# Performance work log

Hardware: AMD Instinct MI355X
Metric: run time of the kernel (lower is better)

## Reference

```python
import jax, jax.numpy as jnp
import numpy as np

MODES = 256
WIDTH = 64
T_HIST = 1
T_FUT = 1
BATCH = 64
S = 8192


def setup_inputs() -> dict:
    key = jax.random.key(0)
    ks = jax.random.split(key, 12)
    scale = 1.0 / (WIDTH * WIDTH)
    inp = {
        "u": jax.random.normal(ks[0], (BATCH, S, T_HIST), dtype=jnp.float32),
        # lifting layer: Linear(T_HIST+1 -> WIDTH), stored [in, out]
        "fc0_w": jax.random.normal(ks[1], (T_HIST + 1, WIDTH), dtype=jnp.float32) * 0.5,
        "fc0_b": jax.random.normal(ks[2], (WIDTH,), dtype=jnp.float32) * 0.1,
        # 4 spectral conv layers, complex weights stored as real/imag parts
        "sw_r": scale * jax.random.uniform(ks[3], (4, WIDTH, WIDTH, MODES), dtype=jnp.float32),
        "sw_i": scale * jax.random.uniform(ks[4], (4, WIDTH, WIDTH, MODES), dtype=jnp.float32),
        # 4 pointwise (1x1 conv) layers: weight [out,in], bias [out]
        "pw_w": jax.random.normal(ks[5], (4, WIDTH, WIDTH), dtype=jnp.float32) * (1.0 / np.sqrt(WIDTH)),
        "pw_b": jax.random.normal(ks[6], (4, WIDTH), dtype=jnp.float32) * 0.1,
        # projection head
        "fc1_w": jax.random.normal(ks[7], (WIDTH, 128), dtype=jnp.float32) * (1.0 / np.sqrt(WIDTH)),
        "fc1_b": jax.random.normal(ks[8], (128,), dtype=jnp.float32) * 0.1,
        "fc2_w": jax.random.normal(ks[9], (128, T_FUT), dtype=jnp.float32) * (1.0 / np.sqrt(128)),
        "fc2_b": jax.random.normal(ks[10], (T_FUT,), dtype=jnp.float32) * 0.1,
    }
    return inp


def _spectral_conv(x, wr, wi):
    # x: [b, c_in, s] real; weights: [c_in, c_out, MODES] (real/imag parts)
    s = x.shape[-1]
    xf = jnp.fft.rfft(x)                     # [b, c_in, s//2+1] complex
    w = wr + 1j * wi
    om = jnp.einsum('bix,iox->box', xf[:, :, :MODES], w)  # [b, c_out, MODES]
    out_ft = jnp.zeros((x.shape[0], wr.shape[1], s // 2 + 1), dtype=om.dtype)
    out_ft = out_ft.at[:, :, :MODES].set(om)
    return jnp.fft.irfft(out_ft, n=s)        # [b, c_out, s] real


def reference(u, fc0_w, fc0_b, sw_r, sw_i, pw_w, pw_b, fc1_w, fc1_b, fc2_w, fc2_b):
    b, s, _ = u.shape
    grid = jnp.broadcast_to(jnp.linspace(0.0, 1.0, s, dtype=u.dtype)[None, :, None], (b, s, 1))
    x = jnp.concatenate([u, grid], axis=-1)              # [b, s, 2]
    x = x @ fc0_w + fc0_b                                # [b, s, W]
    x = jnp.transpose(x, (0, 2, 1))                      # [b, W, s]
    for l in range(4):
        x1 = _spectral_conv(x, sw_r[l], sw_i[l])
        x2 = jnp.einsum('oi,bis->bos', pw_w[l], x) + pw_b[l][None, :, None]
        x = x1 + x2
        if l < 3:
            x = jax.nn.gelu(x, approximate=False)
    x = jnp.transpose(x, (0, 2, 1))                      # [b, s, W]
    x = jax.nn.gelu(x @ fc1_w + fc1_b, approximate=False)
    x = x @ fc2_w + fc2_b                                # [b, s, T_FUT]
    return x
```

## Files before the change

kernel.cpp:

```cpp
#include <hip/hip_runtime.h>
#include <hip/hip_bf16.h>
#include <math.h>

#define BB 64
#define CC 64
#define SS 8192
#define HS 4096
#define NMODE 256
#define KK2 512

typedef __attribute__((ext_vector_type(8))) short short8;
typedef __attribute__((ext_vector_type(16))) float f32x16;

__device__ __forceinline__ float gelu_exact(float v) {
    return 0.5f * v * (1.0f + erff(v * 0.7071067811865476f));
}
__device__ __forceinline__ float b2f(ushort u) {
    return __uint_as_float(((unsigned int)u) << 16);
}
__device__ __forceinline__ ushort f2b(float v) {
    __hip_bfloat16 h = __float2bfloat16(v);
    return *(ushort*)&h;
}
__device__ __forceinline__ void split2(float v, ushort& h, ushort& l) {
    h = f2b(v);
    l = f2b(v - b2f(h));
}
__device__ __forceinline__ int colk(int c) {
    return (c < 256) ? (c & ~1) : (((c - 256) & ~1) | 1);
}

__global__ void build_T1p(ushort* __restrict__ h, ushort* __restrict__ l) {
    int c = blockIdx.x;
    int n = blockIdx.y * 256 + threadIdx.x;
    int k = colk(c), ri = c & 1;
    int m = (n * k) & (SS - 1);
    float th = (float)m * (6.283185307179586476925f / (float)SS);
    float s, co;
    sincosf(th, &s, &co);
    float v = ri ? -s : co;
    ushort hh, ll;
    split2(v, hh, ll);
    h[(size_t)c * HS + n] = hh;
    l[(size_t)c * HS + n] = ll;
}

__global__ void build_T2r(ushort* __restrict__ h, ushort* __restrict__ l) {
    int n = blockIdx.x;
    int c = blockIdx.y * 256 + threadIdx.x;
    int k = colk(c), ri = c & 1;
    int m = (n * k) & (SS - 1);
    float th = (float)m * (6.283185307179586476925f / (float)SS);
    float s, co;
    sincosf(th, &s, &co);
    float v = ri ? -s : co;
    ushort hh, ll;
    split2(v, hh, ll);
    h[(size_t)n * KK2 + c] = hh;
    l[(size_t)n * KK2 + c] = ll;
}

__global__ void zero_xf(float* __restrict__ p) {
    size_t i = ((size_t)blockIdx.x * 256 + threadIdx.x) * 4;
    *(float4*)&p[i] = make_float4(0.f, 0.f, 0.f, 0.f);
}

__global__ void lift_kernel(const float* __restrict__ u, const float* __restrict__ w0,
                            const float* __restrict__ b0, ushort* __restrict__ Eh,
                            ushort* __restrict__ El, ushort* __restrict__ Oh,
                            ushort* __restrict__ Ol) {
    int n = blockIdx.x * 256 + threadIdx.x;
    int c = blockIdx.y;
    int b = blockIdx.z;
    float g1 = (float)n * (1.0f / (float)(SS - 1));
    float g2 = (float)(n + HS) * (1.0f / (float)(SS - 1));
    float v1 = u[b * SS + n] * w0[c] + g1 * w0[CC + c] + b0[c];
    float v2 = u[b * SS + n + HS] * w0[c] + g2 * w0[CC + c] + b0[c];
    float E = v1 + v2, O = v1 - v2;
    ushort hh, ll;
    size_t idx = (size_t)(b * CC + c) * HS + n;
    split2(E, hh, ll);
    Eh[idx] = hh;
    El[idx] = ll;
    split2(O, hh, ll);
    Oh[idx] = hh;
    Ol[idx] = ll;
}

__global__ __launch_bounds__(256, 3) void dft_mfma(
    const ushort* __restrict__ Eh, const ushort* __restrict__ El,
    const ushort* __restrict__ Oh, const ushort* __restrict__ Ol,
    const ushort* __restrict__ t1h, const ushort* __restrict__ t1l,
    float* __restrict__ Xf) {
    __shared__ __align__(16) ushort SM[16384];
    ushort* As_h = SM;
    ushort* As_l = SM + 4096;
    ushort* Bs_h = SM + 8192;
    ushort* Bs_l = SM + 12288;
    const int t = threadIdx.x;
    const int L = blockIdx.x;
    const int gq = L >> 5, j = L & 31;
    const int c0 = (j >> 3) * 128;
    const int m0 = ((gq & 3) * 8 + (j & 7)) * 128;
    const int kz = (gq >> 2) * 1024;
    const ushort* __restrict__ Ahp = (c0 < 256) ? Eh : Oh;
    const ushort* __restrict__ Alp = (c0 < 256) ? El : Ol;
    const int lane = t & 63, w = t >> 6;
    const int wm = (w >> 1) * 64, wn = (w & 1) * 64;
    const int l32 = lane & 31, lh = lane >> 5;
    const int sr = t >> 1, sh = (t & 1) * 16;
    const int g0 = (t & 1) * 2;
    const int d0 = ((g0 + 0) * 128 + sr) * 8;
    const int d1 = ((g0 + 1) * 128 + sr) * 8;

    f32x16 acc[2][2];
#pragma unroll
    for (int i = 0; i < 2; i++)
#pragma unroll
        for (int jj = 0; jj < 2; jj++) acc[i][jj] = (f32x16)0.f;

    const size_t arow = (size_t)(m0 + sr) * HS;
    const size_t brow = (size_t)(c0 + sr) * HS;
    const int kend = kz + 1024;

    short8 a0h, a1h, a0l, a1l, b0h, b1h, b0l, b1l;
    {
        const size_t ga = arow + kz + sh;
        const size_t gb = brow + kz + sh;
        a0h = *(const short8*)&Ahp[ga];
        a1h = *(const short8*)&Ahp[ga + 8];
        a0l = *(const short8*)&Alp[ga];
        a1l = *(const short8*)&Alp[ga + 8];
        b0h = *(const short8*)&t1h[gb];
        b1h = *(const short8*)&t1h[gb + 8];
        b0l = *(const short8*)&t1l[gb];
        b1l = *(const short8*)&t1l[gb + 8];
    }
    for (int kt = kz; kt < kend; kt += 32) {
        __syncthreads();
        *(short8*)&As_h[d0] = a0h;
        *(short8*)&As_h[d1] = a1h;
        *(short8*)&As_l[d0] = a0l;
        *(short8*)&As_l[d1] = a1l;
        *(short8*)&Bs_h[d0] = b0h;
        *(short8*)&Bs_h[d1] = b1h;
        *(short8*)&Bs_l[d0] = b0l;
        *(short8*)&Bs_l[d1] = b1l;
        __syncthreads();
        const int ktn = (kt + 32 < kend) ? kt + 32 : kz;
        const size_t ga = arow + ktn + sh;
        const size_t gb = brow + ktn + sh;
        a0h = *(const short8*)&Ahp[ga];
        a1h = *(const short8*)&Ahp[ga + 8];
        a0l = *(const short8*)&Alp[ga];
        a1l = *(const short8*)&Alp[ga + 8];
        b0h = *(const short8*)&t1h[gb];
        b1h = *(const short8*)&t1h[gb + 8];
        b0l = *(const short8*)&t1l[gb];
        b1l = *(const short8*)&t1l[gb + 8];
#pragma unroll
        for (int s2 = 0; s2 < 2; s2++) {
            const int kg = s2 * 2 + lh;
            short8 ah[2], al[2], bh2[2], bl2[2];
#pragma unroll
            for (int mt = 0; mt < 2; mt++) {
                int off = (kg * 128 + wm + mt * 32 + l32) * 8;
                ah[mt] = *(const short8*)&As_h[off];
                al[mt] = *(const short8*)&As_l[off];
            }
#pragma unroll
            for (int nt = 0; nt < 2; nt++) {
                int off = (kg * 128 + wn + nt * 32 + l32) * 8;
                bh2[nt] = *(const short8*)&Bs_h[off];
                bl2[nt] = *(const short8*)&Bs_l[off];
            }
#pragma unroll
            for (int nt = 0; nt < 2; nt++)
#pragma unroll
                for (int mt = 0; mt < 2; mt++) {
                    acc[mt][nt] = __builtin_amdgcn_mfma_f32_32x32x16_bf16(ah[mt], bh2[nt], acc[mt][nt], 0, 0, 0);
                    acc[mt][nt] = __builtin_amdgcn_mfma_f32_32x32x16_bf16(ah[mt], bl2[nt], acc[mt][nt], 0, 0, 0);
                    acc[mt][nt] = __builtin_amdgcn_mfma_f32_32x32x16_bf16(al[mt], bh2[nt], acc[mt][nt], 0, 0, 0);
                }
        }
    }
#pragma unroll
    for (int mt = 0; mt < 2; mt++)
#pragma unroll
        for (int nt = 0; nt < 2; nt++) {
            int col = c0 + wn + nt * 32 + l32;
#pragma unroll
            for (int reg = 0; reg < 16; reg++) {
                int row = m0 + wm + mt * 32 + (reg & 3) + 8 * (reg >> 2) + 4 * lh;
                atomicAdd(&Xf[(size_t)row * KK2 + col], acc[mt][nt][reg]);
            }
        }
}

__global__ __launch_bounds__(256) void mode_mix(const float* __restrict__ Xf,
                                                const float* __restrict__ swr,
                                                const float* __restrict__ swi,
                                                ushort* __restrict__ omh,
                                                ushort* __restrict__ oml, int l) {
    int k = threadIdx.x;
    int bg = blockIdx.x * 2;
    int og = blockIdx.y * 2;
    const int cp = ((k & 1) << 8) | ((k >> 1) << 1);
    float ar[2][2] = {}, ai[2][2] = {};
#pragma unroll 2
    for (int i = 0; i < CC; i++) {
        float2 x0 = *(const float2*)&Xf[((size_t)(bg + 0) * CC + i) * KK2 + cp];
        float2 x1 = *(const float2*)&Xf[((size_t)(bg + 1) * CC + i) * KK2 + cp];
        size_t wb = ((size_t)(l * CC + i) * CC + og) * NMODE + k;
        float wr0 = swr[wb], wi0 = swi[wb];
        float wr1 = swr[wb + NMODE], wi1 = swi[wb + NMODE];
        ar[0][0] += x0.x * wr0 - x0.y * wi0;
        ai[0][0] += x0.x * wi0 + x0.y * wr0;
        ar[0][1] += x0.x * wr1 - x0.y * wi1;
        ai[0][1] += x0.x * wi1 + x0.y * wr1;
        ar[1][0] += x1.x * wr0 - x1.y * wi0;
        ai[1][0] += x1.x * wi0 + x1.y * wr0;
        ar[1][1] += x1.x * wr1 - x1.y * wi1;
        ai[1][1] += x1.x * wi1 + x1.y * wr1;
    }
    float ck = (k == 0) ? (1.0f / (float)SS) : (2.0f / (float)SS);
#pragma unroll
    for (int b2 = 0; b2 < 2; b2++)
#pragma unroll
        for (int oo = 0; oo < 2; oo++) {
            float re = ar[b2][oo] * ck;
            float im = ai[b2][oo] * ck;
            ushort hr, lr2, hi2, li2;
            split2(re, hr, lr2);
            split2(im, hi2, li2);
            size_t base = ((size_t)(bg + b2) * CC + og + oo) * KK2 + cp;
            *(ushort2*)&omh[base] = make_ushort2(hr, hi2);
            *(ushort2*)&oml[base] = make_ushort2(lr2, li2);
        }
}

__global__ __launch_bounds__(256, 3) void inv_mfma(
    const ushort* __restrict__ omh, const ushort* __restrict__ oml,
    const ushort* __restrict__ t2h, const ushort* __restrict__ t2l,
    const float* __restrict__ pww, const float* __restrict__ pwb,
    ushort* __restrict__ Eh, ushort* __restrict__ El,
    ushort* __restrict__ Oh, ushort* __restrict__ Ol, int l, int gel) {
    __shared__ __align__(16) ushort SM[12288];
    ushort* As_h = SM;
    ushort* As_l = SM + 4096;
    ushort* Bs_h = SM + 8192;
    ushort* Bs_l = SM + 10240;
    const int t = threadIdx.x;
    const int n0 = blockIdx.x * 64;
    const int row0 = blockIdx.y * 128;
    const int lane = t & 63, w = t >> 6;
    const int wm = (w >> 1) * 64, wn = (w & 1) * 32;
    const int l32 = lane & 31, lh = lane >> 5;
    const int sr = t >> 1, sh = (t & 1) * 16;
    const int g0 = (t & 1) * 2;
    const int dA0 = ((g0 + 0) * 128 + sr) * 8;
    const int dA1 = ((g0 + 1) * 128 + sr) * 8;
    const int srB = (t >> 1) & 63;
    const int dB0 = ((g0 + 0) * 64 + srB) * 8;
    const int dB1 = ((g0 + 1) * 64 + srB) * 8;
    const bool doB = t < 128;

    f32x16 aP[2], aQ[2];
#pragma unroll
    for (int i = 0; i < 2; i++) {
        aP[i] = (f32x16)0.f;
        aQ[i] = (f32x16)0.f;
    }

    const size_t arow = (size_t)(row0 + sr) * KK2;
    const size_t brow = (size_t)(n0 + srB) * KK2;

    short8 a0h, a1h, a0l, a1l, b0h, b1h, b0l, b1l;
    {
        const size_t ga = arow + sh;
        a0h = *(const short8*)&omh[ga];
        a1h = *(const short8*)&omh[ga + 8];
        a0l = *(const short8*)&oml[ga];
        a1l = *(const short8*)&oml[ga + 8];
        if (doB) {
            const size_t gb = brow + sh;
            b0h = *(const short8*)&t2h[gb];
            b1h = *(const short8*)&t2h[gb + 8];
            b0l = *(const short8*)&t2l[gb];
            b1l = *(const short8*)&t2l[gb + 8];
        }
    }
#pragma unroll
    for (int half = 0; half < 2; half++) {
        f32x16* acc = half ? aQ : aP;
        for (int hs8 = 0; hs8 < 8; hs8++) {
            const int hs = half * 8 + hs8;
            __syncthreads();
            *(short8*)&As_h[dA0] = a0h;
            *(short8*)&As_h[dA1] = a1h;
            *(short8*)&As_l[dA0] = a0l;
            *(short8*)&As_l[dA1] = a1l;
            if (doB) {
                *(short8*)&Bs_h[dB0] = b0h;
                *(short8*)&Bs_h[dB1] = b1h;
                *(short8*)&Bs_l[dB0] = b0l;
                *(short8*)&Bs_l[dB1] = b1l;
            }
            __syncthreads();
            const int ktn = (hs + 1 < 16) ? (hs + 1) * 32 : 0;
            const size_t ga = arow + ktn + sh;
            a0h = *(const short8*)&omh[ga];
            a1h = *(const short8*)&omh[ga + 8];
            a0l = *(const short8*)&oml[ga];
            a1l = *(const short8*)&oml[ga + 8];
            if (doB) {
                const size_t gb = brow + ktn + sh;
                b0h = *(const short8*)&t2h[gb];
                b1h = *(const short8*)&t2h[gb + 8];
                b0l = *(const short8*)&t2l[gb];
                b1l = *(const short8*)&t2l[gb + 8];
            }
#pragma unroll
            for (int s2 = 0; s2 < 2; s2++) {
                const int kg = s2 * 2 + lh;
                short8 ah[2], al[2];
#pragma unroll
                for (int mt = 0; mt < 2; mt++) {
                    int off = (kg * 128 + wm + mt * 32 + l32) * 8;
                    ah[mt] = *(const short8*)&As_h[off];
                    al[mt] = *(const short8*)&As_l[off];
                }
                const int offb = (kg * 64 + wn + l32) * 8;
                short8 bh = *(const short8*)&Bs_h[offb];
                short8 bl = *(const short8*)&Bs_l[offb];
#pragma unroll
                for (int mt = 0; mt < 2; mt++) {
                    acc[mt] = __builtin_amdgcn_mfma_f32_32x32x16_bf16(ah[mt], bh, acc[mt], 0, 0, 0);
                    acc[mt] = __builtin_amdgcn_mfma_f32_32x32x16_bf16(ah[mt], bl, acc[mt], 0, 0, 0);
                    acc[mt] = __builtin_amdgcn_mfma_f32_32x32x16_bf16(al[mt], bh, acc[mt], 0, 0, 0);
                }
            }
        }
    }
#pragma unroll
    for (int mt = 0; mt < 2; mt++) {
        f32x16 p = aP[mt];
        aP[mt] = p + aQ[mt];
        aQ[mt] = p - aQ[mt];
    }
    const int bsw = w >> 1;
    const int xbs = t >> 7, xi = (t >> 1) & 63, xseg = (t & 1) * 32;
    const size_t xg = (size_t)(row0 + xbs * 64 + xi) * HS + n0 + xseg;
    const ushort* const srcs[4] = {Eh, El, Oh, Ol};
#pragma unroll
    for (int r = 0; r < 4; r++) {
        const ushort* src = srcs[r];
        const bool isO = (r >= 2), isHi = !(r & 1);
        short8 v0 = *(const short8*)&src[xg];
        short8 v1 = *(const short8*)&src[xg + 8];
        short8 v2 = *(const short8*)&src[xg + 16];
        short8 v3 = *(const short8*)&src[xg + 24];
        __syncthreads();
        {
            ushort* d = &SM[xbs * 4608 + xi * 72 + xseg];
            *(short8*)d = v0;
            *(short8*)(d + 8) = v1;
            *(short8*)(d + 16) = v2;
            *(short8*)(d + 24) = v3;
        }
        __syncthreads();
#pragma unroll
        for (int ks = 0; ks < 4; ks++) {
            short8 pah[2], pal[2], pnh[2], pnl[2];
#pragma unroll
            for (int mt = 0; mt < 2; mt++) {
                int o = mt * 32 + l32;
                const float* pp = &pww[(size_t)(l * CC + o) * CC + ks * 16 + lh * 8];
                float4 pa = *(const float4*)pp;
                float4 pb = *(const float4*)(pp + 4);
                float pv[8] = {pa.x, pa.y, pa.z, pa.w, pb.x, pb.y, pb.z, pb.w};
#pragma unroll
                for (int e = 0; e < 8; e++) {
                    ushort h2, l2;
                    split2(0.5f * pv[e], h2, l2);
                    pah[mt][e] = (short)h2;
                    pal[mt][e] = (short)l2;
                    pnh[mt][e] = (short)(h2 ^ 0x8000);
                    pnl[mt][e] = (short)(l2 ^ 0x8000);
                }
            }
            short8 bf;
            const int rb = bsw * 4608 + (ks * 16 + lh * 8) * 72 + wn + l32;
#pragma unroll
            for (int jj = 0; jj < 8; jj++) bf[jj] = (short)SM[rb + jj * 72];
#pragma unroll
            for (int mt = 0; mt < 2; mt++) {
                aP[mt] = __builtin_amdgcn_mfma_f32_32x32x16_bf16(pah[mt], bf, aP[mt], 0, 0, 0);
                aQ[mt] = __builtin_amdgcn_mfma_f32_32x32x16_bf16(isO ? pnh[mt] : pah[mt], bf, aQ[mt], 0, 0, 0);
                if (isHi) {
                    aP[mt] = __builtin_amdgcn_mfma_f32_32x32x16_bf16(pal[mt], bf, aP[mt], 0, 0, 0);
                    aQ[mt] = __builtin_amdgcn_mfma_f32_32x32x16_bf16(isO ? pnl[mt] : pal[mt], bf, aQ[mt], 0, 0, 0);
                }
            }
        }
    }
#pragma unroll
    for (int mt = 0; mt < 2; mt++)
#pragma unroll
        for (int reg = 0; reg < 16; reg++) {
            int roffs = (reg & 3) + 8 * (reg >> 2) + 4 * lh;
            int o = mt * 32 + roffs;
            float bias = pwb[l * CC + o];
            float uu = aP[mt][reg] + bias;
            float vv = aQ[mt][reg] + bias;
            if (gel) {
                uu = gelu_exact(uu);
                vv = gelu_exact(vv);
            }
            float EE = uu + vv, OO = uu - vv;
            ushort h2, l2;
            size_t gg = (size_t)(row0 + wm + mt * 32 + roffs) * HS + n0 + wn + l32;
            split2(EE, h2, l2);
            Eh[gg] = h2;
            El[gg] = l2;
            split2(OO, h2, l2);
            Oh[gg] = h2;
            Ol[gg] = l2;
        }
}

__global__ __launch_bounds__(256) void head_kernel(
    const ushort* __restrict__ Eh, const ushort* __restrict__ El,
    const ushort* __restrict__ Oh, const ushort* __restrict__ Ol,
    const float* __restrict__ w1, const float* __restrict__ b1,
    const float* __restrict__ w2, const float* __restrict__ b2,
    float* __restrict__ out) {
    __shared__ float Xs[64][64];
    __shared__ float W1s[64][128];
    __shared__ float part[4][64];
    int b = blockIdx.y;
    int n0 = blockIdx.x * 64;
    int tid = threadIdx.x;
    const float sgn = (n0 < HS) ? 1.0f : -1.0f;
    const int nc = n0 & (HS - 1);
    {
        int c = tid >> 2, nq = tid & 3;
        size_t gx = (size_t)(b * CC + c) * HS + nc + nq * 16;
        short8 eh0 = *(const short8*)&Eh[gx], eh1 = *(const short8*)&Eh[gx + 8];
        short8 el0 = *(const short8*)&El[gx], el1 = *(const short8*)&El[gx + 8];
        short8 oh0 = *(const short8*)&Oh[gx], oh1 = *(const short8*)&Oh[gx + 8];
        short8 ol0 = *(const short8*)&Ol[gx], ol1 = *(const short8*)&Ol[gx + 8];
#pragma unroll
        for (int e = 0; e < 8; e++) {
            float e0 = b2f((ushort)eh0[e]) + b2f((ushort)el0[e]);
            float o0 = b2f((ushort)oh0[e]) + b2f((ushort)ol0[e]);
            float e1 = b2f((ushort)eh1[e]) + b2f((ushort)el1[e]);
            float o1 = b2f((ushort)oh1[e]) + b2f((ushort)ol1[e]);
            Xs[c][nq * 16 + e] = 0.5f * (e0 + sgn * o0);
            Xs[c][nq * 16 + 8 + e] = 0.5f * (e1 + sgn * o1);
        }
    }
    float* w1flat = &W1s[0][0];
#pragma unroll
    for (int q = 0; q < 8; q++) {
        int off = q * 1024 + tid * 4;
        *(float4*)&w1flat[off] = *(const float4*)&w1[off];
    }
    __syncthreads();
    int nn = tid & 63, jg = tid >> 6;
    float h[32];
#pragma unroll
    for (int jj = 0; jj < 32; jj++) h[jj] = b1[jg * 32 + jj];
    for (int c = 0; c < 64; c++) {
        float xv = Xs[c][nn];
#pragma unroll
        for (int jj = 0; jj < 32; jj++)
            h[jj] = fmaf(xv, W1s[c][jg * 32 + jj], h[jj]);
    }
    float p = 0.f;
#pragma unroll
    for (int jj = 0; jj < 32; jj++)
        p = fmaf(gelu_exact(h[jj]), w2[jg * 32 + jj], p);
    part[jg][nn] = p;
    __syncthreads();
    if (tid < 64) {
        float v = part[0][tid] + part[1][tid] + part[2][tid] + part[3][tid] + b2[0];
        out[b * SS + n0 + tid] = v;
    }
}

extern "C" void kernel_launch(void* const* d_in, const int* in_sizes, int n_in,
                              void* d_out, int out_size, void* d_ws, size_t ws_size,
                              hipStream_t stream) {
    (void)in_sizes; (void)n_in; (void)out_size; (void)ws_size;
    const float* u = (const float*)d_in[0];
    const float* fc0_w = (const float*)d_in[1];
    const float* fc0_b = (const float*)d_in[2];
    const float* sw_r = (const float*)d_in[3];
    const float* sw_i = (const float*)d_in[4];
    const float* pw_w = (const float*)d_in[5];
    const float* pw_b = (const float*)d_in[6];
    const float* fc1_w = (const float*)d_in[7];
    const float* fc1_b = (const float*)d_in[8];
    const float* fc2_w = (const float*)d_in[9];
    const float* fc2_b = (const float*)d_in[10];
    float* out = (float*)d_out;

    char* ws = (char*)d_ws;
    ushort* Eh = (ushort*)ws;
    ushort* El = (ushort*)(ws + 33554432);
    ushort* Oh = (ushort*)(ws + 67108864);
    ushort* Ol = (ushort*)(ws + 100663296);
    ushort* t1h = (ushort*)(ws + 134217728);
    ushort* t1l = (ushort*)(ws + 138412032);
    ushort* t2h = (ushort*)(ws + 142606336);
    ushort* t2l = (ushort*)(ws + 146800640);
    ushort* omh = (ushort*)(ws + 150994944);
    ushort* oml = (ushort*)(ws + 155189248);
    float* Xf = (float*)(ws + 159383552);

    build_T1p<<<dim3(KK2, HS / 256), 256, 0, stream>>>(t1h, t1l);
    build_T2r<<<dim3(HS, KK2 / 256), 256, 0, stream>>>(t2h, t2l);
    lift_kernel<<<dim3(HS / 256, CC, BB), 256, 0, stream>>>(u, fc0_w, fc0_b, Eh, El,
                                                            Oh, Ol);
    for (int l = 0; l < 4; l++) {
        zero_xf<<<dim3(2048), 256, 0, stream>>>(Xf);
        dft_mfma<<<dim3(512), 256, 0, stream>>>(Eh, El, Oh, Ol, t1h, t1l, Xf);
        mode_mix<<<dim3(BB / 2, CC / 2), 256, 0, stream>>>(Xf, sw_r, sw_i, omh, oml, l);
        inv_mfma<<<dim3(HS / 64, 32), 256, 0, stream>>>(
            omh, oml, t2h, t2l, pw_w, pw_b, Eh, El, Oh, Ol, l, (l < 3) ? 1 : 0);
    }
    head_kernel<<<dim3(SS / 64, BB), 256, 0, stream>>>(Eh, El, Oh, Ol, fc1_w, fc1_b,
                                                       fc2_w, fc2_b, out);
}
```

Measured before the change: 1.447 ms.

## Move projection head onto bf16x3 MFMA and share E/O tiles across both halves

The head kernel's fc1 matmul moves from scalar FMA loops to split-bf16 MFMA, with a pre-transposed, pre-halved, split copy of fc1_w built once per call. Each block now reads one E/O tile and produces outputs for both position n and n+HS using linearity (E±O). This halves the grid and cuts redundant global loads of the even/odd buffers. The cost is an extra small setup kernel, shuffle-based reductions across lanes, and bf16x3 rounding instead of plain fp32 FMA.

```diff
diff --git a/kernel.cpp b/kernel.cpp
--- a/kernel.cpp
+++ b/kernel.cpp
@@ -58,6 +58,16 @@
     split2(v, hh, ll);
     h[(size_t)n * KK2 + c] = hh;
     l[(size_t)n * KK2 + c] = ll;
+}
+
+__global__ void build_W1T(const float* __restrict__ w1, ushort* __restrict__ h,
+                          ushort* __restrict__ l) {
+    int j = blockIdx.x;
+    int c = threadIdx.x;
+    ushort hh, ll;
+    split2(0.5f * w1[c * 128 + j], hh, ll);
+    h[j * 64 + c] = hh;
+    l[j * 64 + c] = ll;
 }
 
 __global__ void zero_xf(float* __restrict__ p) {
@@ -432,60 +442,104 @@
 __global__ __launch_bounds__(256) void head_kernel(
     const ushort* __restrict__ Eh, const ushort* __restrict__ El,
     const ushort* __restrict__ Oh, const ushort* __restrict__ Ol,
-    const float* __restrict__ w1, const float* __restrict__ b1,
-    const float* __restrict__ w2, const float* __restrict__ b2,
-    float* __restrict__ out) {
-    __shared__ float Xs[64][64];
-    __shared__ float W1s[64][128];
-    __shared__ float part[4][64];
-    int b = blockIdx.y;
-    int n0 = blockIdx.x * 64;
-    int tid = threadIdx.x;
-    const float sgn = (n0 < HS) ? 1.0f : -1.0f;
-    const int nc = n0 & (HS - 1);
+    const ushort* __restrict__ w1th, const ushort* __restrict__ w1tl,
+    const float* __restrict__ b1, const float* __restrict__ w2,
+    const float* __restrict__ b2, float* __restrict__ out) {
+    __shared__ __align__(16) ushort SM[18432];
+    ushort* EhT = SM;
+    ushort* ElT = SM + 4608;
+    ushort* OhT = SM + 9216;
+    ushort* OlT = SM + 13824;
+    __shared__ float Ru[4][64], Rv[4][64];
+    const int b = blockIdx.y;
+    const int n0 = blockIdx.x * 64;
+    const int t = threadIdx.x;
+    const int lane = t & 63, w = t >> 6;
+    const int l32 = lane & 31, lh = lane >> 5;
     {
-        int c = tid >> 2, nq = tid & 3;
-        size_t gx = (size_t)(b * CC + c) * HS + nc + nq * 16;
-        short8 eh0 = *(const short8*)&Eh[gx], eh1 = *(const short8*)&Eh[gx + 8];
-        short8 el0 = *(const short8*)&El[gx], el1 = *(const short8*)&El[gx + 8];
-        short8 oh0 = *(const short8*)&Oh[gx], oh1 = *(const short8*)&Oh[gx + 8];
-        short8 ol0 = *(const short8*)&Ol[gx], ol1 = *(const short8*)&Ol[gx + 8];
-#pragma unroll
-        for (int e = 0; e < 8; e++) {
-            float e0 = b2f((ushort)eh0[e]) + b2f((ushort)el0[e]);
-            float o0 = b2f((ushort)oh0[e]) + b2f((ushort)ol0[e]);
-            float e1 = b2f((ushort)eh1[e]) + b2f((ushort)el1[e]);
-            float o1 = b2f((ushort)oh1[e]) + b2f((ushort)ol1[e]);
-            Xs[c][nq * 16 + e] = 0.5f * (e0 + sgn * o0);
-            Xs[c][nq * 16 + 8 + e] = 0.5f * (e1 + sgn * o1);
-        }
-    }
-    float* w1flat = &W1s[0][0];
-#pragma unroll
-    for (int q = 0; q < 8; q++) {
-        int off = q * 1024 + tid * 4;
-        *(float4*)&w1flat[off] = *(const float4*)&w1[off];
+        const int c = t >> 2, ns = (t & 3) * 16;
+        const size_t g = (size_t)(b * CC + c) * HS + n0 + ns;
+        const ushort* const srcs[4] = {Eh, El, Oh, Ol};
+        ushort* const dsts[4] = {EhT, ElT, OhT, OlT};
+#pragma unroll
+        for (int r = 0; r < 4; r++) {
+            short8 v0 = *(const short8*)&srcs[r][g];
+            short8 v1 = *(const short8*)&srcs[r][g + 8];
+            ushort* d = dsts[r];
+#pragma unroll
+            for (int e = 0; e < 8; e++) {
+                d[(ns + e) * 72 + c] = (ushort)v0[e];
+                d[(ns + 8 + e) * 72 + c] = (ushort)v1[e];
+            }
+        }
+    }
+    const int jbase = w * 32;
+    short8 Bh[4], Bl[4];
+#pragma unroll
+    for (int ks = 0; ks < 4; ks++) {
+        const size_t gw = (size_t)(jbase + l32) * 64 + ks * 16 + lh * 8;
+        Bh[ks] = *(const short8*)&w1th[gw];
+        Bl[ks] = *(const short8*)&w1tl[gw];
     }
     __syncthreads();
-    int nn = tid & 63, jg = tid >> 6;
-    float h[32];
-#pragma unroll
-    for (int jj = 0; jj < 32; jj++) h[jj] = b1[jg * 32 + jj];
-    for (int c = 0; c < 64; c++) {
-        float xv = Xs[c][nn];
-#pragma unroll
-        for (int jj = 0; jj < 32; jj++)
-            h[jj] = fmaf(xv, W1s[c][jg * 32 + jj], h[jj]);
-    }
-    float p = 0.f;
-#pragma unroll
-    for (int jj = 0; jj < 32; jj++)
-        p = fmaf(gelu_exact(h[jj]), w2[jg * 32 + jj], p);
-    part[jg][nn] = p;
+    f32x16 aE[2], aO[2];
+#pragma unroll
+    for (int i = 0; i < 2; i++) {
+        aE[i] = (f32x16)0.f;
+        aO[i] = (f32x16)0.f;
+    }
+#pragma unroll
+    for (int ks = 0; ks < 4; ks++) {
+#pragma unroll
+        for (int mt = 0; mt < 2; mt++) {
+            const int r = (mt * 32 + l32) * 72 + ks * 16 + lh * 8;
+            short8 Ah = *(const short8*)&EhT[r];
+            short8 Al = *(const short8*)&ElT[r];
+            aE[mt] = __builtin_amdgcn_mfma_f32_32x32x16_bf16(Ah, Bh[ks], aE[mt], 0, 0, 0);
+            aE[mt] = __builtin_amdgcn_mfma_f32_32x32x16_bf16(Ah, Bl[ks], aE[mt], 0, 0, 0);
+            aE[mt] = __builtin_amdgcn_mfma_f32_32x32x16_bf16(Al, Bh[ks], aE[mt], 0, 0, 0);
+            Ah = *(const short8*)&OhT[r];
+            Al = *(const short8*)&OlT[r];
+            aO[mt] = __builtin_amdgcn_mfma_f32_32x32x16_bf16(Ah, Bh[ks], aO[mt], 0, 0, 0);
+            aO[mt] = __builtin_amdgcn_mfma_f32_32x32x16_bf16(Ah, Bl[ks], aO[mt], 0, 0, 0);
+            aO[mt] = __builtin_amdgcn_mfma_f32_32x32x16_bf16(Al, Bh[ks], aO[mt], 0, 0, 0);
+        }
+    }
+    const float b1v = b1[jbase + l32];
+    const float w2v = w2[jbase + l32];
+    float pu[32], pv[32];
+#pragma unroll
+    for (int mt = 0; mt < 2; mt++)
+#pragma unroll
+        for (int reg = 0; reg < 16; reg++) {
+            float hu = aE[mt][reg] + aO[mt][reg] + b1v;
+            float hv = aE[mt][reg] - aO[mt][reg] + b1v;
+            pu[mt * 16 + reg] = gelu_exact(hu) * w2v;
+            pv[mt * 16 + reg] = gelu_exact(hv) * w2v;
+        }
+#pragma unroll
+    for (int m = 1; m <= 16; m <<= 1)
+#pragma unroll
+        for (int i = 0; i < 32; i++) {
+            pu[i] += __shfl_xor(pu[i], m, 64);
+            pv[i] += __shfl_xor(pv[i], m, 64);
+        }
+    if (l32 == 0) {
+#pragma unroll
+        for (int mt = 0; mt < 2; mt++)
+#pragma unroll
+            for (int reg = 0; reg < 16; reg++) {
+                int row = mt * 32 + (reg & 3) + 8 * (reg >> 2) + 4 * lh;
+                Ru[w][row] = pu[mt * 16 + reg];
+                Rv[w][row] = pv[mt * 16 + reg];
+            }
+    }
     __syncthreads();
-    if (tid < 64) {
-        float v = part[0][tid] + part[1][tid] + part[2][tid] + part[3][tid] + b2[0];
-        out[b * SS + n0 + tid] = v;
+    if (t < 64) {
+        float su = Ru[0][t] + Ru[1][t] + Ru[2][t] + Ru[3][t] + b2[0];
+        float sv = Rv[0][t] + Rv[1][t] + Rv[2][t] + Rv[3][t] + b2[0];
+        out[(size_t)b * SS + n0 + t] = su;
+        out[(size_t)b * SS + n0 + t + HS] = sv;
     }
 }
 
@@ -518,9 +572,12 @@
     ushort* omh = (ushort*)(ws + 150994944);
     ushort* oml = (ushort*)(ws + 155189248);
     float* Xf = (float*)(ws + 159383552);
+    ushort* w1th = (ushort*)(ws + 167772160);
+    ushort* w1tl = (ushort*)(ws + 167788544);
 
     build_T1p<<<dim3(KK2, HS / 256), 256, 0, stream>>>(t1h, t1l);
     build_T2r<<<dim3(HS, KK2 / 256), 256, 0, stream>>>(t2h, t2l);
+    build_W1T<<<dim3(128), 64, 0, stream>>>(fc1_w, w1th, w1tl);
     lift_kernel<<<dim3(HS / 256, CC, BB), 256, 0, stream>>>(u, fc0_w, fc0_b, Eh, El,
                                                             Oh, Ol);
     for (int l = 0; l < 4; l++) {
@@ -530,6 +587,6 @@
         inv_mfma<<<dim3(HS / 64, 32), 256, 0, stream>>>(
             omh, oml, t2h, t2l, pw_w, pw_b, Eh, El, Oh, Ol, l, (l < 3) ? 1 : 0);
     }
-    head_kernel<<<dim3(SS / 64, BB), 256, 0, stream>>>(Eh, El, Oh, Ol, fc1_w, fc1_b,
-                                                       fc2_w, fc2_b, out);
-}
+    head_kernel<<<dim3(HS / 64, BB), 256, 0, stream>>>(Eh, El, Oh, Ol, w1th, w1tl,
+                                                       fc1_b, fc2_w, fc2_b, out);
+}
```

New measurement: 1.511 ms. 4.4% more time.
